# Optimization experiments

Hardware: AMD Instinct MI355X
Metric: run time of the kernel (lower is better)

Reference implementation:

```python
import jax, jax.numpy as jnp
import numpy as np
from jax import lax

B, H, D, S, T, V = 128, 512, 512, 80, 28, 30000

def setup_inputs() -> dict:
    key = jax.random.key(0)
    ks = jax.random.split(key, 20)
    s = 0.02
    return {
        "encoder_last_hidden_state": jax.random.normal(ks[0], (1, B, H), jnp.float32),
        "encoder_output": jax.random.normal(ks[1], (B, S, H), jnp.float32),
        "targets": jax.random.randint(ks[2], (B, T), 0, V),
        "embedding": jax.random.normal(ks[3], (V, D), jnp.float32) * s,
        "W1": jax.random.normal(ks[4], (H, 2 * H), jnp.float32) * s,
        "b1": jnp.zeros((H,), jnp.float32),
        "W2": jax.random.normal(ks[5], (H, H), jnp.float32) * s,
        "b2": jnp.zeros((H,), jnp.float32),
        "W3": jax.random.normal(ks[6], (H, H), jnp.float32) * s,
        "b3": jnp.zeros((H,), jnp.float32),
        "W4": jax.random.normal(ks[7], (H, H), jnp.float32) * s,
        "b4": jnp.zeros((H,), jnp.float32),
        "w_att": jax.random.normal(ks[8], (1, H), jnp.float32) * s,
        "W_ih": jax.random.normal(ks[9], (4 * H, H + D), jnp.float32) * s,
        "W_hh": jax.random.normal(ks[10], (4 * H, H), jnp.float32) * s,
        "b_ih": jnp.zeros((4 * H,), jnp.float32),
        "b_hh": jnp.zeros((4 * H,), jnp.float32),
        "W_out": jax.random.normal(ks[11], (V, H), jnp.float32) * s,
        "b_out": jnp.zeros((V,), jnp.float32),
    }


def reference(encoder_last_hidden_state, encoder_output, targets, embedding,
              W1, b1, W2, b2, W3, b3, W4, b4, w_att,
              W_ih, W_hh, b_ih, b_hh, W_out, b_out):
    # Deterministic teacher forcing (threshold > max of random.uniform for large tr_steps).
    h = encoder_last_hidden_state[0]          # (B, H)
    c = jnp.zeros_like(h)
    emb = embedding[targets[:, :-1]]          # (B, T-1, D)
    xs = jnp.swapaxes(emb, 0, 1)              # (T-1, B, D)

    def step(carry, x):
        h, c = carry
        # --- attention (4 stacked linears, no nonlinearity, as in source) ---
        hs = jnp.broadcast_to(h[:, None, :], encoder_output.shape)  # (B,S,H)
        m = jnp.concatenate([encoder_output, hs], axis=-1)          # (B,S,2H)
        a = m @ W1.T + b1
        a = a @ W2.T + b2
        a = a @ W3.T + b3
        a = a @ W4.T + b4
        scores = jnp.einsum('bsh,h->bs', a, w_att[0])               # (B,S)
        att = jax.nn.softmax(scores, axis=1)
        ctx = jnp.einsum('bs,bsh->bh', att, encoder_output)         # (B,H)
        # --- single-step LSTM (PyTorch gate order i,f,g,o) ---
        li = jnp.concatenate([x, ctx], axis=-1)                     # (B, D+H)
        gates = li @ W_ih.T + h @ W_hh.T + b_ih + b_hh
        i_, f_, g_, o_ = jnp.split(gates, 4, axis=-1)
        c2 = jax.nn.sigmoid(f_) * c + jax.nn.sigmoid(i_) * jnp.tanh(g_)
        h2 = jax.nn.sigmoid(o_) * jnp.tanh(c2)
        logits = h2 @ W_out.T + b_out                               # (B,V)
        return (h2, c2), logits

    _, logits = lax.scan(step, (h, c), xs)    # (T-1, B, V)
    seq_logProb = jnp.swapaxes(logits, 0, 1)  # (B, T-1, V)
    seq_predictions = jnp.argmax(seq_logProb, axis=-1)
    return seq_logProb, seq_predictions
```

## Files before the change

### kernel.cpp

```cpp
#include <hip/hip_runtime.h>
#include <math.h>

#define BB 128
#define HH 512
#define SS 80
#define NT 27
#define VV 30000
#define NBLK 469

typedef short bf16x8 __attribute__((ext_vector_type(8)));
typedef float f32x4  __attribute__((ext_vector_type(4)));
typedef unsigned long long u64;

#define OFF_WE     0
#define OFF_CTX    512
#define OFF_H      (OFF_CTX + BB*HH)
#define OFF_C      (OFF_H + BB*HH)
#define OFF_GATES  (OFF_C + BB*HH)
#define OFF_SLOTS  (OFF_GATES + BB*2048)
#define OFF_GCTX   (OFF_SLOTS + 2*NT*BB)
#define OFF_GIN    (OFF_GCTX + BB*2048)
#define WS_FULL_FLOATS (OFF_GIN + NT*BB*2048)
#define OFF_WHI    WS_FULL_FLOATS
#define OFF_WLO    (OFF_WHI + VV*256)
#define OFF_HHI    (OFF_WLO + VV*256)
#define OFF_HLO    (OFF_HHI + BB*256)
#define OFF_PART   (OFF_HLO + BB*256)
#define WS_MFMA_FLOATS (OFF_PART + NT*NBLK*BB*2)

__device__ __forceinline__ unsigned long long pack_max(float v, int n) {
    unsigned u = __float_as_uint(v);
    unsigned key = (u & 0x80000000u) ? ~u : (u | 0x80000000u);
    return ((unsigned long long)key << 32) | (unsigned)(~(unsigned)n);
}

__device__ __forceinline__ unsigned short bf16_rne(float x) {
    unsigned u = __float_as_uint(x);
    unsigned r = (u + 0x7fffu + ((u >> 16) & 1u)) >> 16;
    return (unsigned short)r;
}
__device__ __forceinline__ float bf16f(unsigned short h) {
    return __uint_as_float((unsigned)h << 16);
}
__device__ __forceinline__ u64 shfl_xor_u64(u64 v, int m) {
    unsigned lo = (unsigned)v, hi = (unsigned)(v >> 32);
    lo = __shfl_xor(lo, m, 64);
    hi = __shfl_xor(hi, m, 64);
    return ((u64)hi << 32) | lo;
}

__global__ void k_init(const float* __restrict__ elhs, float* __restrict__ h,
                       float* __restrict__ c, unsigned long long* __restrict__ slots) {
    int i = blockIdx.x * blockDim.x + threadIdx.x;
    if (i < BB * HH) { h[i] = elhs[i]; c[i] = 0.f; }
    if (i < NT * BB) slots[i] = 0ull;
}

__global__ __launch_bounds__(256) void k_we(const float* __restrict__ W1, const float* __restrict__ W2,
                                            const float* __restrict__ W3, const float* __restrict__ W4,
                                            const float* __restrict__ watt, float* __restrict__ we_out) {
    __shared__ float v[HH], v2[HH];
    int tid = threadIdx.x;
    for (int k = tid; k < HH; k += 256) v[k] = watt[k];
    __syncthreads();
    const float* Ws[3] = {W4, W3, W2};
    for (int l = 0; l < 3; ++l) {
        const float* W = Ws[l];
        for (int k = tid; k < HH; k += 256) {
            float s = 0.f;
            for (int j = 0; j < HH; ++j) s += v[j] * W[j * HH + k];
            v2[k] = s;
        }
        __syncthreads();
        for (int k = tid; k < HH; k += 256) v[k] = v2[k];
        __syncthreads();
    }
    for (int k = tid; k < HH; k += 256) {
        float s = 0.f;
        for (int j = 0; j < HH; ++j) s += v[j] * W1[j * (2 * HH) + k];
        we_out[k] = s;
    }
}

__global__ __launch_bounds__(256) void k_attn(const float* __restrict__ eo, const float* __restrict__ we,
                                              float* __restrict__ ctx) {
    __shared__ float wsm[HH];
    __shared__ float sc[SS];
    int b = blockIdx.x, tid = threadIdx.x;
    for (int k = tid; k < HH; k += 256) wsm[k] = we[k];
    __syncthreads();
    int wid = tid >> 6, lane = tid & 63;
    const float* eob = eo + (size_t)b * SS * HH;
    for (int s = wid; s < SS; s += 4) {
        float p = 0.f;
        for (int k = lane; k < HH; k += 64) p += eob[s * HH + k] * wsm[k];
        for (int off = 32; off > 0; off >>= 1) p += __shfl_down(p, off, 64);
        if (lane == 0) sc[s] = p;
    }
    __syncthreads();
    if (wid == 0) {
        float a = (lane < SS) ? sc[lane] : -INFINITY;
        float bv = (lane + 64 < SS) ? sc[lane + 64] : -INFINITY;
        float m = fmaxf(a, bv);
        for (int off = 32; off > 0; off >>= 1) m = fmaxf(m, __shfl_down(m, off, 64));
        m = __shfl(m, 0, 64);
        float e0 = (lane < SS) ? expf(a - m) : 0.f;
        float e1 = (lane + 64 < SS) ? expf(bv - m) : 0.f;
        float ssum = e0 + e1;
        for (int off = 32; off > 0; off >>= 1) ssum += __shfl_down(ssum, off, 64);
        ssum = __shfl(ssum, 0, 64);
        float inv = 1.f / ssum;
        if (lane < SS) sc[lane] = e0 * inv;
        if (lane + 64 < SS) sc[lane + 64] = e1 * inv;
    }
    __syncthreads();
    for (int hh = tid; hh < HH; hh += 256) {
        float acc = 0.f;
        for (int s = 0; s < SS; ++s) acc += sc[s] * eob[s * HH + hh];
        ctx[b * HH + hh] = acc;
    }
}

__global__ __launch_bounds__(256) void k_gin(const float* __restrict__ emb, const int* __restrict__ targets,
                                             const float* __restrict__ Wih, float* __restrict__ gin) {
    const int n0 = blockIdx.x * 64, m0 = blockIdx.y * 64;
    __shared__ __align__(16) float As[32][68];
    __shared__ __align__(16) float Bs[32][68];
    int tid = threadIdx.x;
    int tx = tid & 15, ty = tid >> 4;
    float acc[4][4] = {};
    for (int kt = 0; kt < 512; kt += 32) {
        #pragma unroll
        for (int i = 0; i < 2; ++i) {
            int idx = tid + i * 256;
            int mm = idx >> 3, k4 = (idx & 7) * 4;
            int m = m0 + mm;
            int t = m >> 7, b = m & 127;
            int row = targets[b * 28 + t];
            float4 v = *(const float4*)(emb + (size_t)row * 512 + kt + k4);
            As[k4 + 0][mm] = v.x; As[k4 + 1][mm] = v.y; As[k4 + 2][mm] = v.z; As[k4 + 3][mm] = v.w;
        }
        #pragma unroll
        for (int i = 0; i < 2; ++i) {
            int idx = tid + i * 256;
            int nn = idx >> 3, k4 = (idx & 7) * 4;
            float4 v = *(const float4*)(Wih + (size_t)(n0 + nn) * 1024 + kt + k4);
            Bs[k4 + 0][nn] = v.x; Bs[k4 + 1][nn] = v.y; Bs[k4 + 2][nn] = v.z; Bs[k4 + 3][nn] = v.w;
        }
        __syncthreads();
        #pragma unroll
        for (int k = 0; k < 32; ++k) {
            float4 a = *(const float4*)&As[k][ty * 4];
            float4 b4 = *(const float4*)&Bs[k][tx * 4];
            float av[4] = {a.x, a.y, a.z, a.w}, bv[4] = {b4.x, b4.y, b4.z, b4.w};
            #pragma unroll
            for (int i = 0; i < 4; ++i)
                #pragma unroll
                for (int j = 0; j < 4; ++j) acc[i][j] += av[i] * bv[j];
        }
        __syncthreads();
    }
    #pragma unroll
    for (int i = 0; i < 4; ++i) {
        int m = m0 + ty * 4 + i;
        float4 o = {acc[i][0], acc[i][1], acc[i][2], acc[i][3]};
        *(float4*)(gin + (size_t)m * 2048 + n0 + tx * 4) = o;
    }
}

__global__ __launch_bounds__(256) void k_gctx(const float* __restrict__ ctx, const float* __restrict__ Wih,
                                              const float* __restrict__ bih, const float* __restrict__ bhh,
                                              float* __restrict__ gctx) {
    const int n0 = blockIdx.x * 64, m0 = blockIdx.y * 32;
    __shared__ __align__(16) float As[32][36];
    __shared__ __align__(16) float Bs[32][68];
    int tid = threadIdx.x;
    int tx = tid & 15, ty = tid >> 4;
    float acc[2][4] = {};
    for (int kt = 0; kt < 512; kt += 32) {
        {
            int mm = tid >> 3, k4 = (tid & 7) * 4;
            float4 v = *(const float4*)(ctx + (size_t)(m0 + mm) * 512 + kt + k4);
            As[k4 + 0][mm] = v.x; As[k4 + 1][mm] = v.y; As[k4 + 2][mm] = v.z; As[k4 + 3][mm] = v.w;
        }
        #pragma unroll
        for (int i = 0; i < 2; ++i) {
            int idx = tid + i * 256;
            int nn = idx >> 3, k4 = (idx & 7) * 4;
            float4 v = *(const float4*)(Wih + (size_t)(n0 + nn) * 1024 + 512 + kt + k4);
            Bs[k4 + 0][nn] = v.x; Bs[k4 + 1][nn] = v.y; Bs[k4 + 2][nn] = v.z; Bs[k4 + 3][nn] = v.w;
        }
        __syncthreads();
        #pragma unroll
        for (int k = 0; k < 32; ++k) {
            float a0 = As[k][ty * 2], a1 = As[k][ty * 2 + 1];
            float4 b4 = *(const float4*)&Bs[k][tx * 4];
            float bv[4] = {b4.x, b4.y, b4.z, b4.w};
            #pragma unroll
            for (int j = 0; j < 4; ++j) { acc[0][j] += a0 * bv[j]; acc[1][j] += a1 * bv[j]; }
        }
        __syncthreads();
    }
    #pragma unroll
    for (int i = 0; i < 2; ++i) {
        int b = m0 + ty * 2 + i;
        int n = n0 + tx * 4;
        float4 o = {acc[i][0] + bih[n] + bhh[n], acc[i][1] + bih[n + 1] + bhh[n + 1],
                    acc[i][2] + bih[n + 2] + bhh[n + 2], acc[i][3] + bih[n + 3] + bhh[n + 3]};
        *(float4*)(gctx + (size_t)b * 2048 + n) = o;
    }
}

template <bool FULL>
__global__ __launch_bounds__(256) void k_gates(const float* __restrict__ emb, const int* __restrict__ targets,
                                               const float* __restrict__ ctx, const float* __restrict__ h,
                                               const float* __restrict__ Wih, const float* __restrict__ Whh,
                                               const float* __restrict__ bih, const float* __restrict__ bhh,
                                               const float* __restrict__ gin, const float* __restrict__ gctx,
                                               float* __restrict__ gates, int t) {
    const int n0 = blockIdx.x * 64, m0 = blockIdx.y * 32;
    __shared__ __align__(16) float As[32][36];
    __shared__ __align__(16) float Bs[32][68];
    int tid = threadIdx.x;
    int tx = tid & 15, ty = tid >> 4;
    float acc[2][4] = {};
    const int KTOT = FULL ? 1536 : 512;
    for (int kt = 0; kt < KTOT; kt += 32) {
        {
            int mm = tid >> 3, k4 = (tid & 7) * 4;
            int b = m0 + mm, k = kt + k4;
            const float* src;
            if (FULL) {
                if (k < 512) { int row = targets[b * 28 + t]; src = emb + (size_t)row * 512 + k; }
                else if (k < 1024) src = ctx + (size_t)b * 512 + (k - 512);
                else src = h + (size_t)b * 512 + (k - 1024);
            } else {
                src = h + (size_t)b * 512 + k;
            }
            float4 v = *(const float4*)src;
            As[k4 + 0][mm] = v.x; As[k4 + 1][mm] = v.y; As[k4 + 2][mm] = v.z; As[k4 + 3][mm] = v.w;
        }
        #pragma unroll
        for (int i = 0; i < 2; ++i) {
            int idx = tid + i * 256;
            int nn = idx >> 3, k4 = (idx & 7) * 4;
            int n = n0 + nn, k = kt + k4;
            const float* src;
            if (FULL) {
                if (k < 1024) src = Wih + (size_t)n * 1024 + k;
                else src = Whh + (size_t)n * 512 + (k - 1024);
            } else {
                src = Whh + (size_t)n * 512 + k;
            }
            float4 v = *(const float4*)src;
            Bs[k4 + 0][nn] = v.x; Bs[k4 + 1][nn] = v.y; Bs[k4 + 2][nn] = v.z; Bs[k4 + 3][nn] = v.w;
        }
        __syncthreads();
        #pragma unroll
        for (int k = 0; k < 32; ++k) {
            float a0 = As[k][ty * 2], a1 = As[k][ty * 2 + 1];
            float4 b4 = *(const float4*)&Bs[k][tx * 4];
            float bv[4] = {b4.x, b4.y, b4.z, b4.w};
            #pragma unroll
            for (int j = 0; j < 4; ++j) { acc[0][j] += a0 * bv[j]; acc[1][j] += a1 * bv[j]; }
        }
        __syncthreads();
    }
    #pragma unroll
    for (int i = 0; i < 2; ++i) {
        int b = m0 + ty * 2 + i;
        int n = n0 + tx * 4;
        float base[4];
        if (FULL) {
            #pragma unroll
            for (int j = 0; j < 4; ++j) base[j] = bih[n + j] + bhh[n + j];
        } else {
            const float* g1 = gin + ((size_t)t * BB + b) * 2048 + n;
            const float* g2 = gctx + (size_t)b * 2048 + n;
            #pragma unroll
            for (int j = 0; j < 4; ++j) base[j] = g1[j] + g2[j];
        }
        float4 o = {acc[i][0] + base[0], acc[i][1] + base[1], acc[i][2] + base[2], acc[i][3] + base[3]};
        *(float4*)(gates + (size_t)b * 2048 + n) = o;
    }
}

__global__ void k_lstm(const float* __restrict__ gates, float* __restrict__ h, float* __restrict__ c) {
    int idx = blockIdx.x * blockDim.x + threadIdx.x;
    int b = idx >> 9, j = idx & 511;
    const float* g = gates + (size_t)b * 2048;
    float iv = g[j], fv = g[512 + j], gv = g[1024 + j], ov = g[1536 + j];
    float si = 1.f / (1.f + expf(-iv));
    float sf = 1.f / (1.f + expf(-fv));
    float so = 1.f / (1.f + expf(-ov));
    float c2 = sf * c[idx] + si * tanhf(gv);
    c[idx] = c2;
    h[idx] = so * tanhf(c2);
}

__global__ void k_lstm2(const float* __restrict__ gates, float* __restrict__ h, float* __restrict__ c,
                        unsigned short* __restrict__ hHi, unsigned short* __restrict__ hLo) {
    int idx = blockIdx.x * blockDim.x + threadIdx.x;
    int b = idx >> 9, j = idx & 511;
    const float* g = gates + (size_t)b * 2048;
    float iv = g[j], fv = g[512 + j], gv = g[1024 + j], ov = g[1536 + j];
    float si = 1.f / (1.f + expf(-iv));
    float sf = 1.f / (1.f + expf(-fv));
    float so = 1.f / (1.f + expf(-ov));
    float c2 = sf * c[idx] + si * tanhf(gv);
    c[idx] = c2;
    float hv = so * tanhf(c2);
    h[idx] = hv;
    unsigned short hh = bf16_rne(hv);
    hHi[idx] = hh;
    hLo[idx] = bf16_rne(hv - bf16f(hh));
}

__global__ __launch_bounds__(256) void k_split(const float* __restrict__ src, unsigned short* __restrict__ hi,
                                               unsigned short* __restrict__ lo, int n4) {
    int i = blockIdx.x * 256 + threadIdx.x;
    if (i >= n4) return;
    float4 v = ((const float4*)src)[i];
    unsigned short h0 = bf16_rne(v.x), h1 = bf16_rne(v.y), h2 = bf16_rne(v.z), h3 = bf16_rne(v.w);
    ushort4 hv = {h0, h1, h2, h3};
    ushort4 lv = {bf16_rne(v.x - bf16f(h0)), bf16_rne(v.y - bf16f(h1)),
                  bf16_rne(v.z - bf16f(h2)), bf16_rne(v.w - bf16f(h3))};
    ((ushort4*)hi)[i] = hv;
    ((ushort4*)lo)[i] = lv;
}

__global__ __launch_bounds__(256, 2) void k_vproj2(
    const unsigned short* __restrict__ hHi, const unsigned short* __restrict__ hLo,
    const unsigned short* __restrict__ wHi, const unsigned short* __restrict__ wLo,
    const float* __restrict__ bout, float* __restrict__ out,
    u64* __restrict__ part, int t)
{
    const int tid = threadIdx.x;
    const int lane = tid & 63;
    const int wv = tid >> 6;
    const int wm = wv >> 1;
    const int wn = wv & 1;
    const int g = lane >> 4;
    const int q = lane & 15;
    const int n0 = blockIdx.x * 64;

    int aIdx[4];
    int bIdx[2], colv[2];
    float bo[2];
    #pragma unroll
    for (int mt = 0; mt < 4; ++mt) aIdx[mt] = (wm * 64 + mt * 16 + q) * 512 + g * 8;
    #pragma unroll
    for (int nt = 0; nt < 2; ++nt) {
        int col = n0 + wn * 32 + nt * 16 + q;
        colv[nt] = col;
        int cc = col < VV ? col : (VV - 1);
        bIdx[nt] = cc * 512 + g * 8;
        bo[nt] = bout[cc];
    }

    f32x4 zero = {0.f, 0.f, 0.f, 0.f};
    f32x4 acc[4][2];
    #pragma unroll
    for (int mt = 0; mt < 4; ++mt)
        #pragma unroll
        for (int nt = 0; nt < 2; ++nt) acc[mt][nt] = zero;

#define LOADK(K, AH, AL, BH, BL) do {                                    \
        _Pragma("unroll") for (int mt_ = 0; mt_ < 4; ++mt_) {            \
            AH[mt_] = *(const bf16x8*)(hHi + aIdx[mt_] + (K));           \
            AL[mt_] = *(const bf16x8*)(hLo + aIdx[mt_] + (K)); }         \
        _Pragma("unroll") for (int nt_ = 0; nt_ < 2; ++nt_) {            \
            BH[nt_] = *(const bf16x8*)(wHi + bIdx[nt_] + (K));           \
            BL[nt_] = *(const bf16x8*)(wLo + bIdx[nt_] + (K)); }         \
    } while (0)

#define MM(AH, AL, BH, BL) do {                                                                     \
        _Pragma("unroll") for (int mt_ = 0; mt_ < 4; ++mt_)                                         \
        _Pragma("unroll") for (int nt_ = 0; nt_ < 2; ++nt_) {                                       \
            acc[mt_][nt_] = __builtin_amdgcn_mfma_f32_16x16x32_bf16(AH[mt_], BH[nt_], acc[mt_][nt_], 0, 0, 0); \
            acc[mt_][nt_] = __builtin_amdgcn_mfma_f32_16x16x32_bf16(AH[mt_], BL[nt_], acc[mt_][nt_], 0, 0, 0); \
            acc[mt_][nt_] = __builtin_amdgcn_mfma_f32_16x16x32_bf16(AL[mt_], BH[nt_], acc[mt_][nt_], 0, 0, 0); \
        }                                                                                           \
    } while (0)

    bf16x8 aH0[4], aL0[4], bH0[2], bL0[2];
    bf16x8 aH1[4], aL1[4], bH1[2], bL1[2];
    LOADK(0, aH0, aL0, bH0, bL0);
    #pragma unroll
    for (int s = 0; s < 16; s += 2) {
        if (s + 1 < 16) LOADK((s + 1) * 32, aH1, aL1, bH1, bL1);
        MM(aH0, aL0, bH0, bL0);
        if (s + 2 < 16) LOADK((s + 2) * 32, aH0, aL0, bH0, bL0);
        if (s + 1 < 16) MM(aH1, aL1, bH1, bL1);
    }
#undef LOADK
#undef MM

    __shared__ u64 red[BB][2];
    #pragma unroll
    for (int mt = 0; mt < 4; ++mt) {
        #pragma unroll
        for (int r = 0; r < 4; ++r) {
            int row = wm * 64 + mt * 16 + 4 * g + r;
            u64 pk = 0ull;
            #pragma unroll
            for (int nt = 0; nt < 2; ++nt) {
                float v = acc[mt][nt][r] + bo[nt];
                int col = colv[nt];
                if (col < VV) out[((size_t)row * NT + t) * VV + col] = v;
                u64 p2 = pack_max(v, col);
                if (p2 > pk) pk = p2;
            }
            #pragma unroll
            for (int m_ = 1; m_ < 16; m_ <<= 1) {
                u64 o = shfl_xor_u64(pk, m_);
                if (o > pk) pk = o;
            }
            if (q == 0) red[row][wn] = pk;
        }
    }
    __syncthreads();
    if (tid < BB) {
        u64 a = red[tid][0], b2 = red[tid][1];
        part[((size_t)t * NBLK + blockIdx.x) * BB + tid] = a > b2 ? a : b2;
    }
}

__global__ __launch_bounds__(256) void k_vproj(const float* __restrict__ h, const float* __restrict__ Wout,
                                               const float* __restrict__ bout, float* __restrict__ out,
                                               unsigned long long* __restrict__ slots, int t) {
    const int n0 = blockIdx.x * 64, m0 = blockIdx.y * 64;
    __shared__ __align__(16) float As[32][68];
    __shared__ __align__(16) float Bs[32][68];
    __shared__ unsigned long long red[64][17];
    int tid = threadIdx.x;
    int tx = tid & 15, ty = tid >> 4;
    float acc[4][4] = {};
    for (int kt = 0; kt < 512; kt += 32) {
        #pragma unroll
        for (int i = 0; i < 2; ++i) {
            int idx = tid + i * 256;
            int mm = idx >> 3, k4 = (idx & 7) * 4;
            float4 v = *(const float4*)(h + (size_t)(m0 + mm) * 512 + kt + k4);
            As[k4 + 0][mm] = v.x; As[k4 + 1][mm] = v.y; As[k4 + 2][mm] = v.z; As[k4 + 3][mm] = v.w;
        }
        #pragma unroll
        for (int i = 0; i < 2; ++i) {
            int idx = tid + i * 256;
            int nn = idx >> 3, k4 = (idx & 7) * 4;
            int n = n0 + nn; if (n >= VV) n = VV - 1;
            float4 v = *(const float4*)(Wout + (size_t)n * 512 + kt + k4);
            Bs[k4 + 0][nn] = v.x; Bs[k4 + 1][nn] = v.y; Bs[k4 + 2][nn] = v.z; Bs[k4 + 3][nn] = v.w;
        }
        __syncthreads();
        #pragma unroll
        for (int k = 0; k < 32; ++k) {
            float4 a = *(const float4*)&As[k][ty * 4];
            float4 b4 = *(const float4*)&Bs[k][tx * 4];
            float av[4] = {a.x, a.y, a.z, a.w}, bv[4] = {b4.x, b4.y, b4.z, b4.w};
            #pragma unroll
            for (int i = 0; i < 4; ++i)
                #pragma unroll
                for (int j = 0; j < 4; ++j) acc[i][j] += av[i] * bv[j];
        }
        __syncthreads();
    }
    #pragma unroll
    for (int i = 0; i < 4; ++i) {
        int m = m0 + ty * 4 + i;
        int n = n0 + tx * 4;
        float vals[4];
        #pragma unroll
        for (int j = 0; j < 4; ++j) vals[j] = acc[i][j] + ((n + j < VV) ? bout[n + j] : 0.f);
        size_t ob = ((size_t)m * NT + t) * VV;
        if (n + 3 < VV) {
            float4 o = {vals[0], vals[1], vals[2], vals[3]};
            *(float4*)(out + ob + n) = o;
        } else {
            for (int j = 0; j < 4; ++j) if (n + j < VV) out[ob + n + j] = vals[j];
        }
        unsigned long long p = 0ull;
        #pragma unroll
        for (int j = 0; j < 4; ++j)
            if (n + j < VV) {
                unsigned long long pk = pack_max(vals[j], n + j);
                if (pk > p) p = pk;
            }
        red[ty * 4 + i][tx] = p;
    }
    __syncthreads();
    if (tid < 64) {
        unsigned long long best = red[tid][0];
        #pragma unroll
        for (int j = 1; j < 16; ++j) { unsigned long long q = red[tid][j]; if (q > best) best = q; }
        atomicMax(&slots[t * BB + (m0 + tid)], best);
    }
}

__global__ void k_final(const unsigned long long* __restrict__ slots, float* __restrict__ out) {
    int i = blockIdx.x * blockDim.x + threadIdx.x;
    if (i >= NT * BB) return;
    int t = i / BB, b = i % BB;
    unsigned idx = ~(unsigned)(slots[i] & 0xffffffffull);
    out[(size_t)BB * NT * VV + (size_t)b * NT + t] = (float)idx;
}

__global__ void k_final2(const u64* __restrict__ part, float* __restrict__ out) {
    int i = blockIdx.x * blockDim.x + threadIdx.x;
    if (i >= NT * BB) return;
    int t = i >> 7, b = i & 127;
    const u64* p = part + (size_t)t * NBLK * BB + b;
    u64 best = 0ull;
    for (int nb = 0; nb < NBLK; ++nb) {
        u64 v = p[(size_t)nb * BB];
        if (v > best) best = v;
    }
    unsigned idx = ~(unsigned)(best & 0xffffffffull);
    out[(size_t)BB * NT * VV + (size_t)b * NT + t] = (float)idx;
}

extern "C" void kernel_launch(void* const* d_in, const int* in_sizes, int n_in,
                              void* d_out, int out_size, void* d_ws, size_t ws_size,
                              hipStream_t stream) {
    const float* elhs    = (const float*)d_in[0];
    const float* eo      = (const float*)d_in[1];
    const int*   targets = (const int*)d_in[2];
    const float* emb     = (const float*)d_in[3];
    const float* W1      = (const float*)d_in[4];
    const float* W2      = (const float*)d_in[6];
    const float* W3      = (const float*)d_in[8];
    const float* W4      = (const float*)d_in[10];
    const float* watt    = (const float*)d_in[12];
    const float* Wih     = (const float*)d_in[13];
    const float* Whh     = (const float*)d_in[14];
    const float* bih     = (const float*)d_in[15];
    const float* bhh     = (const float*)d_in[16];
    const float* Wout    = (const float*)d_in[17];
    const float* bout    = (const float*)d_in[18];

    float* out = (float*)d_out;
    float* ws  = (float*)d_ws;
    float* we    = ws + OFF_WE;
    float* ctx   = ws + OFF_CTX;
    float* h     = ws + OFF_H;
    float* c     = ws + OFF_C;
    float* gates = ws + OFF_GATES;
    unsigned long long* slots = (unsigned long long*)(ws + OFF_SLOTS);
    float* gctx  = ws + OFF_GCTX;
    float* gin   = ws + OFF_GIN;
    unsigned short* wHi = (unsigned short*)(ws + OFF_WHI);
    unsigned short* wLo = (unsigned short*)(ws + OFF_WLO);
    unsigned short* hHi = (unsigned short*)(ws + OFF_HHI);
    unsigned short* hLo = (unsigned short*)(ws + OFF_HLO);
    u64* part = (u64*)(ws + OFF_PART);

    const bool use_gin  = ws_size >= (size_t)WS_FULL_FLOATS * sizeof(float);
    const bool use_mfma = ws_size >= (size_t)WS_MFMA_FLOATS * sizeof(float);

    k_init<<<256, 256, 0, stream>>>(elhs, h, c, slots);
    k_we<<<1, 256, 0, stream>>>(W1, W2, W3, W4, watt, we);
    k_attn<<<BB, 256, 0, stream>>>(eo, we, ctx);
    if (use_mfma)
        k_split<<<(VV * 128 + 255) / 256, 256, 0, stream>>>(Wout, wHi, wLo, VV * 128);
    if (use_gin) {
        k_gin<<<dim3(32, 54), 256, 0, stream>>>(emb, targets, Wih, gin);
        k_gctx<<<dim3(32, 4), 256, 0, stream>>>(ctx, Wih, bih, bhh, gctx);
    }
    for (int t = 0; t < NT; ++t) {
        if (use_gin)
            k_gates<false><<<dim3(32, 4), 256, 0, stream>>>(emb, targets, ctx, h, Wih, Whh, bih, bhh, gin, gctx, gates, t);
        else
            k_gates<true><<<dim3(32, 4), 256, 0, stream>>>(emb, targets, ctx, h, Wih, Whh, bih, bhh, gin, gctx, gates, t);
        if (use_mfma) {
            k_lstm2<<<128, 512, 0, stream>>>(gates, h, c, hHi, hLo);
            k_vproj2<<<NBLK, 256, 0, stream>>>(hHi, hLo, wHi, wLo, bout, out, part, t);
        } else {
            k_lstm<<<128, 512, 0, stream>>>(gates, h, c);
            k_vproj<<<dim3(469, 2), 256, 0, stream>>>(h, Wout, bout, out, slots, t);
        }
    }
    if (use_mfma)
        k_final2<<<14, 256, 0, stream>>>(part, out);
    else
        k_final<<<14, 256, 0, stream>>>(slots, out);
}
```

Baseline: 2.850 ms.

## Batch vocab projection across all timesteps into one MFMA launch

Stores every step's split bf16 hidden state in a per-timestep buffer, then runs the output projection for all 27 steps in a single large kernel instead of one per step. This moves the large W_out GEMM off the serial recurrence, removing 27 small launches and letting many more blocks run at once. It needs a larger workspace and falls back to the old paths when the workspace is too small. The per-step kernel's software-pipelined double-buffered loads are also replaced by a simple loop.

```diff
diff --git a/kernel.cpp b/kernel.cpp
--- a/kernel.cpp
+++ b/kernel.cpp
@@ -27,6 +27,12 @@
 #define OFF_HLO    (OFF_HHI + BB*256)
 #define OFF_PART   (OFF_HLO + BB*256)
 #define WS_MFMA_FLOATS (OFF_PART + NT*NBLK*BB*2)
+#define OFF_WHI_B   WS_FULL_FLOATS
+#define OFF_WLO_B   (OFF_WHI_B + VV*256)
+#define OFF_HALLHI  (OFF_WLO_B + VV*256)
+#define OFF_HALLLO  (OFF_HALLHI + NT*BB*256)
+#define OFF_PART_B  (OFF_HALLLO + NT*BB*256)
+#define WS_BATCH_FLOATS (OFF_PART_B + NT*NBLK*BB*2)
 
 __device__ __forceinline__ unsigned long long pack_max(float v, int n) {
     unsigned u = __float_as_uint(v);
@@ -329,6 +335,91 @@
     ((ushort4*)lo)[i] = lv;
 }
 
+__global__ __launch_bounds__(256, 3) void k_vprojB(
+    const unsigned short* __restrict__ hAllHi, const unsigned short* __restrict__ hAllLo,
+    const unsigned short* __restrict__ wHi, const unsigned short* __restrict__ wLo,
+    const float* __restrict__ bout, float* __restrict__ out,
+    u64* __restrict__ part)
+{
+    const int bid = blockIdx.x;
+    const int nblk = bid / NT;
+    const int t = bid - nblk * NT;
+    const int n0 = nblk * 64;
+    const int tid = threadIdx.x;
+    const int lane = tid & 63;
+    const int wv = tid >> 6;
+    const int g = lane >> 4;
+    const int q = lane & 15;
+
+    int aIdx[2];
+    int bIdx[4], colv[4];
+    float bo[4];
+    #pragma unroll
+    for (int mt = 0; mt < 2; ++mt)
+        aIdx[mt] = ((t * BB) + wv * 32 + mt * 16 + q) * 512 + g * 8;
+    #pragma unroll
+    for (int nt = 0; nt < 4; ++nt) {
+        int col = n0 + nt * 16 + q;
+        colv[nt] = col;
+        int cc = col < VV ? col : (VV - 1);
+        bIdx[nt] = cc * 512 + g * 8;
+        bo[nt] = bout[cc];
+    }
+
+    f32x4 zero = {0.f, 0.f, 0.f, 0.f};
+    f32x4 acc[2][4];
+    #pragma unroll
+    for (int mt = 0; mt < 2; ++mt)
+        #pragma unroll
+        for (int nt = 0; nt < 4; ++nt) acc[mt][nt] = zero;
+
+    for (int s = 0; s < 16; ++s) {
+        const int K = s * 32;
+        bf16x8 aH[2], aL[2], bH[4], bL[4];
+        #pragma unroll
+        for (int mt = 0; mt < 2; ++mt) {
+            aH[mt] = *(const bf16x8*)(hAllHi + aIdx[mt] + K);
+            aL[mt] = *(const bf16x8*)(hAllLo + aIdx[mt] + K);
+        }
+        #pragma unroll
+        for (int nt = 0; nt < 4; ++nt) {
+            bH[nt] = *(const bf16x8*)(wHi + bIdx[nt] + K);
+            bL[nt] = *(const bf16x8*)(wLo + bIdx[nt] + K);
+        }
+        #pragma unroll
+        for (int mt = 0; mt < 2; ++mt)
+            #pragma unroll
+            for (int nt = 0; nt < 4; ++nt) {
+                acc[mt][nt] = __builtin_amdgcn_mfma_f32_16x16x32_bf16(aH[mt], bH[nt], acc[mt][nt], 0, 0, 0);
+                acc[mt][nt] = __builtin_amdgcn_mfma_f32_16x16x32_bf16(aH[mt], bL[nt], acc[mt][nt], 0, 0, 0);
+                acc[mt][nt] = __builtin_amdgcn_mfma_f32_16x16x32_bf16(aL[mt], bH[nt], acc[mt][nt], 0, 0, 0);
+            }
+    }
+
+    #pragma unroll
+    for (int mt = 0; mt < 2; ++mt) {
+        #pragma unroll
+        for (int r = 0; r < 4; ++r) {
+            int row = wv * 32 + mt * 16 + 4 * g + r;
+            u64 pk = 0ull;
+            #pragma unroll
+            for (int nt = 0; nt < 4; ++nt) {
+                float v = acc[mt][nt][r] + bo[nt];
+                int col = colv[nt];
+                if (col < VV) out[((size_t)row * NT + t) * VV + col] = v;
+                u64 p2 = pack_max(v, col);
+                if (p2 > pk) pk = p2;
+            }
+            #pragma unroll
+            for (int m_ = 1; m_ < 16; m_ <<= 1) {
+                u64 o = shfl_xor_u64(pk, m_);
+                if (o > pk) pk = o;
+            }
+            if (q == 0) part[((size_t)t * NBLK + nblk) * BB + row] = pk;
+        }
+    }
+}
+
 __global__ __launch_bounds__(256, 2) void k_vproj2(
     const unsigned short* __restrict__ hHi, const unsigned short* __restrict__ hLo,
     const unsigned short* __restrict__ wHi, const unsigned short* __restrict__ wLo,
@@ -365,36 +456,28 @@
         #pragma unroll
         for (int nt = 0; nt < 2; ++nt) acc[mt][nt] = zero;
 
-#define LOADK(K, AH, AL, BH, BL) do {                                    \
-        _Pragma("unroll") for (int mt_ = 0; mt_ < 4; ++mt_) {            \
-            AH[mt_] = *(const bf16x8*)(hHi + aIdx[mt_] + (K));           \
-            AL[mt_] = *(const bf16x8*)(hLo + aIdx[mt_] + (K)); }         \
-        _Pragma("unroll") for (int nt_ = 0; nt_ < 2; ++nt_) {            \
-            BH[nt_] = *(const bf16x8*)(wHi + bIdx[nt_] + (K));           \
-            BL[nt_] = *(const bf16x8*)(wLo + bIdx[nt_] + (K)); }         \
-    } while (0)
-
-#define MM(AH, AL, BH, BL) do {                                                                     \
-        _Pragma("unroll") for (int mt_ = 0; mt_ < 4; ++mt_)                                         \
-        _Pragma("unroll") for (int nt_ = 0; nt_ < 2; ++nt_) {                                       \
-            acc[mt_][nt_] = __builtin_amdgcn_mfma_f32_16x16x32_bf16(AH[mt_], BH[nt_], acc[mt_][nt_], 0, 0, 0); \
-            acc[mt_][nt_] = __builtin_amdgcn_mfma_f32_16x16x32_bf16(AH[mt_], BL[nt_], acc[mt_][nt_], 0, 0, 0); \
-            acc[mt_][nt_] = __builtin_amdgcn_mfma_f32_16x16x32_bf16(AL[mt_], BH[nt_], acc[mt_][nt_], 0, 0, 0); \
-        }                                                                                           \
-    } while (0)
-
-    bf16x8 aH0[4], aL0[4], bH0[2], bL0[2];
-    bf16x8 aH1[4], aL1[4], bH1[2], bL1[2];
-    LOADK(0, aH0, aL0, bH0, bL0);
-    #pragma unroll
-    for (int s = 0; s < 16; s += 2) {
-        if (s + 1 < 16) LOADK((s + 1) * 32, aH1, aL1, bH1, bL1);
-        MM(aH0, aL0, bH0, bL0);
-        if (s + 2 < 16) LOADK((s + 2) * 32, aH0, aL0, bH0, bL0);
-        if (s + 1 < 16) MM(aH1, aL1, bH1, bL1);
-    }
-#undef LOADK
-#undef MM
+    for (int s = 0; s < 16; ++s) {
+        const int K = s * 32;
+        bf16x8 aH[4], aL[4], bH[2], bL[2];
+        #pragma unroll
+        for (int mt = 0; mt < 4; ++mt) {
+            aH[mt] = *(const bf16x8*)(hHi + aIdx[mt] + K);
+            aL[mt] = *(const bf16x8*)(hLo + aIdx[mt] + K);
+        }
+        #pragma unroll
+        for (int nt = 0; nt < 2; ++nt) {
+            bH[nt] = *(const bf16x8*)(wHi + bIdx[nt] + K);
+            bL[nt] = *(const bf16x8*)(wLo + bIdx[nt] + K);
+        }
+        #pragma unroll
+        for (int mt = 0; mt < 4; ++mt)
+            #pragma unroll
+            for (int nt = 0; nt < 2; ++nt) {
+                acc[mt][nt] = __builtin_amdgcn_mfma_f32_16x16x32_bf16(aH[mt], bH[nt], acc[mt][nt], 0, 0, 0);
+                acc[mt][nt] = __builtin_amdgcn_mfma_f32_16x16x32_bf16(aH[mt], bL[nt], acc[mt][nt], 0, 0, 0);
+                acc[mt][nt] = __builtin_amdgcn_mfma_f32_16x16x32_bf16(aL[mt], bH[nt], acc[mt][nt], 0, 0, 0);
+            }
+    }
 
     __shared__ u64 red[BB][2];
     #pragma unroll
@@ -548,39 +631,62 @@
     unsigned long long* slots = (unsigned long long*)(ws + OFF_SLOTS);
     float* gctx  = ws + OFF_GCTX;
     float* gin   = ws + OFF_GIN;
-    unsigned short* wHi = (unsigned short*)(ws + OFF_WHI);
-    unsigned short* wLo = (unsigned short*)(ws + OFF_WLO);
-    unsigned short* hHi = (unsigned short*)(ws + OFF_HHI);
-    unsigned short* hLo = (unsigned short*)(ws + OFF_HLO);
-    u64* part = (u64*)(ws + OFF_PART);
-
-    const bool use_gin  = ws_size >= (size_t)WS_FULL_FLOATS * sizeof(float);
-    const bool use_mfma = ws_size >= (size_t)WS_MFMA_FLOATS * sizeof(float);
+
+    const bool use_gin   = ws_size >= (size_t)WS_FULL_FLOATS * sizeof(float);
+    const bool use_batch = ws_size >= (size_t)WS_BATCH_FLOATS * sizeof(float);
+    const bool use_mfma  = !use_batch && ws_size >= (size_t)WS_MFMA_FLOATS * sizeof(float);
 
     k_init<<<256, 256, 0, stream>>>(elhs, h, c, slots);
     k_we<<<1, 256, 0, stream>>>(W1, W2, W3, W4, watt, we);
     k_attn<<<BB, 256, 0, stream>>>(eo, we, ctx);
-    if (use_mfma)
-        k_split<<<(VV * 128 + 255) / 256, 256, 0, stream>>>(Wout, wHi, wLo, VV * 128);
     if (use_gin) {
         k_gin<<<dim3(32, 54), 256, 0, stream>>>(emb, targets, Wih, gin);
         k_gctx<<<dim3(32, 4), 256, 0, stream>>>(ctx, Wih, bih, bhh, gctx);
     }
-    for (int t = 0; t < NT; ++t) {
-        if (use_gin)
-            k_gates<false><<<dim3(32, 4), 256, 0, stream>>>(emb, targets, ctx, h, Wih, Whh, bih, bhh, gin, gctx, gates, t);
-        else
-            k_gates<true><<<dim3(32, 4), 256, 0, stream>>>(emb, targets, ctx, h, Wih, Whh, bih, bhh, gin, gctx, gates, t);
-        if (use_mfma) {
+
+    if (use_batch) {
+        unsigned short* wHi    = (unsigned short*)(ws + OFF_WHI_B);
+        unsigned short* wLo    = (unsigned short*)(ws + OFF_WLO_B);
+        unsigned short* hAllHi = (unsigned short*)(ws + OFF_HALLHI);
+        unsigned short* hAllLo = (unsigned short*)(ws + OFF_HALLLO);
+        u64* part = (u64*)(ws + OFF_PART_B);
+        k_split<<<(VV * 128 + 255) / 256, 256, 0, stream>>>(Wout, wHi, wLo, VV * 128);
+        for (int t = 0; t < NT; ++t) {
+            if (use_gin)
+                k_gates<false><<<dim3(32, 4), 256, 0, stream>>>(emb, targets, ctx, h, Wih, Whh, bih, bhh, gin, gctx, gates, t);
+            else
+                k_gates<true><<<dim3(32, 4), 256, 0, stream>>>(emb, targets, ctx, h, Wih, Whh, bih, bhh, gin, gctx, gates, t);
+            k_lstm2<<<128, 512, 0, stream>>>(gates, h, c,
+                                             hAllHi + (size_t)t * BB * 512,
+                                             hAllLo + (size_t)t * BB * 512);
+        }
+        k_vprojB<<<NBLK * NT, 256, 0, stream>>>(hAllHi, hAllLo, wHi, wLo, bout, out, part);
+        k_final2<<<14, 256, 0, stream>>>(part, out);
+    } else if (use_mfma) {
+        unsigned short* wHi = (unsigned short*)(ws + OFF_WHI);
+        unsigned short* wLo = (unsigned short*)(ws + OFF_WLO);
+        unsigned short* hHi = (unsigned short*)(ws + OFF_HHI);
+        unsigned short* hLo = (unsigned short*)(ws + OFF_HLO);
+        u64* part = (u64*)(ws + OFF_PART);
+        k_split<<<(VV * 128 + 255) / 256, 256, 0, stream>>>(Wout, wHi, wLo, VV * 128);
+        for (int t = 0; t < NT; ++t) {
+            if (use_gin)
+                k_gates<false><<<dim3(32, 4), 256, 0, stream>>>(emb, targets, ctx, h, Wih, Whh, bih, bhh, gin, gctx, gates, t);
+            else
+                k_gates<true><<<dim3(32, 4), 256, 0, stream>>>(emb, targets, ctx, h, Wih, Whh, bih, bhh, gin, gctx, gates, t);
             k_lstm2<<<128, 512, 0, stream>>>(gates, h, c, hHi, hLo);
             k_vproj2<<<NBLK, 256, 0, stream>>>(hHi, hLo, wHi, wLo, bout, out, part, t);
-        } else {
+        }
+        k_final2<<<14, 256, 0, stream>>>(part, out);
+    } else {
+        for (int t = 0; t < NT; ++t) {
+            if (use_gin)
+                k_gates<false><<<dim3(32, 4), 256, 0, stream>>>(emb, targets, ctx, h, Wih, Whh, bih, bhh, gin, gctx, gates, t);
+            else
+                k_gates<true><<<dim3(32, 4), 256, 0, stream>>>(emb, targets, ctx, h, Wih, Whh, bih, bhh, gin, gctx, gates, t);
             k_lstm<<<128, 512, 0, stream>>>(gates, h, c);
             k_vproj<<<dim3(469, 2), 256, 0, stream>>>(h, Wout, bout, out, slots, t);
         }
-    }
-    if (use_mfma)
-        k_final2<<<14, 256, 0, stream>>>(part, out);
-    else
         k_final<<<14, 256, 0, stream>>>(slots, out);
-}
+    }
+}
```

New measurement: 2.526 ms. 11.4% less time.
